# Kernel optimization log

Measured on AMD Instinct MI355X. Metric: run time of the kernel, lower is better.

The kernel has to match this reference:

```python
import jax, jax.numpy as jnp
import numpy as np

T, B, A, OBS = 128, 16, 32, 256
K, NACT, HID = 3, 9, 32


def setup_inputs() -> dict:
    key = jax.random.key(0)
    ks = jax.random.split(key, 12)
    sc = 0.1  # small init scale for stability
    d = {}
    d["x"] = jax.random.normal(ks[0], (T, B, A, OBS), jnp.float32)
    d["done"] = jax.random.randint(ks[1], (T, B), 0, 2, jnp.int32)
    d["actions"] = jax.random.randint(ks[2], (T, B, A, K), 0, NACT, jnp.int32)
    d["W1"] = sc * jax.random.normal(ks[3], (128, OBS), jnp.float32)
    d["b1"] = jnp.zeros((128,), jnp.float32)
    d["W2"] = sc * jax.random.normal(ks[4], (128, 128), jnp.float32)
    d["b2"] = jnp.zeros((128,), jnp.float32)
    d["W3"] = sc * jax.random.normal(ks[5], (64, 128), jnp.float32)
    d["b3"] = jnp.zeros((64,), jnp.float32)
    d["Wih"] = sc * jax.random.normal(ks[6], (4 * HID, 64), jnp.float32)
    d["Whh"] = sc * jax.random.normal(ks[7], (4 * HID, HID), jnp.float32)
    d["bih"] = jnp.zeros((4 * HID,), jnp.float32)
    d["bhh"] = jnp.zeros((4 * HID,), jnp.float32)
    d["Wh"] = sc * jax.random.normal(ks[8], (K, NACT, HID), jnp.float32)
    d["bh"] = jnp.zeros((K, NACT), jnp.float32)
    d["h0"] = jnp.zeros((B * A, HID), jnp.float32)
    d["c0"] = jnp.zeros((B * A, HID), jnp.float32)
    return d


def _forward(x, done, actions, W1, b1, W2, b2, W3, b3,
             Wih, Whh, bih, bhh, Wh, bh, h0, c0):
    # MLP trunk: n_obs -> 128 -> 128 -> 64 (tanh, tanh, linear)
    z = jnp.tanh(x @ W1.T + b1)
    z = jnp.tanh(z @ W2.T + b2)
    z = z @ W3.T + b3                       # [T, B, A, 64]
    zf = z.reshape(T, B * A, 64)
    # done[t] repeated per agent (repeat_interleave along batch*agent axis)
    done_f = jnp.repeat(done.astype(x.dtype), A, axis=1)  # [T, B*A]

    def step(carry, inp):
        h, c = carry
        zt, dt = inp                        # [B*A,64], [B*A]
        mask = (1.0 - dt)[:, None]
        h = h * mask
        c = c * mask
        gates = zt @ Wih.T + bih + h @ Whh.T + bhh  # [B*A, 4H]
        i, f, g, o = jnp.split(gates, 4, axis=-1)   # PyTorch gate order i,f,g,o
        i, f, o = jax.nn.sigmoid(i), jax.nn.sigmoid(f), jax.nn.sigmoid(o)
        g = jnp.tanh(g)
        c = f * c + i * g
        h = o * jnp.tanh(c)
        return (h, c), h

    (_, _), ys = jax.lax.scan(step, (h0, c0), (zf, done_f))
    y = ys.reshape(T, B, A, HID)
    # multi-head categorical logits: stacked heads [K, NACT, HID]
    logits = jnp.einsum('tbah,knh->tbakn', y, Wh) + bh  # [T,B,A,K,NACT]
    lp = jax.nn.log_softmax(logits, axis=-1)
    entropies = -jnp.sum(jnp.exp(lp) * lp, axis=-1)     # [T,B,A,K]
    alp = jnp.take_along_axis(lp, actions[..., None], axis=-1)[..., 0]  # [T,B,A,K]
    logprobs = jnp.prod(alp, axis=-1)  # faithful: product of per-head log-probs
    return logprobs, entropies


def reference(x, done, actions, W1, b1, W2, b2, W3, b3,
              Wih, Whh, bih, bhh, Wh, bh, h0, c0):
    logprobs, entropies = _forward(x, done, actions, W1, b1, W2, b2, W3, b3,
                                   Wih, Whh, bih, bhh, Wh, bh, h0, c0)
    return actions, logprobs, entropies
```

## Files before the change

kernel.cpp:

```cpp
#include <hip/hip_runtime.h>
#include <math.h>

namespace {
constexpr int Tn = 128, Bn = 16, An = 32, OBS = 256, Kh = 3, NACT = 9, HID = 32;
constexpr int TBA = Tn * Bn * An;
constexpr int BA  = Bn * An;
constexpr int OUT_LP  = TBA * Kh;
constexpr int OUT_ENT = TBA * Kh + TBA;
constexpr int NCHUNK = 32;
constexpr int CHUNKW = Tn / NCHUNK;

constexpr int W1_OFF  = 0;
constexpr int W2_OFF  = 32768;
constexpr int W3_OFF  = 49152;
constexpr int WIH_OFF = 57344;
constexpr int W16_TOT = 65536;

typedef __fp16   pk16x2 __attribute__((ext_vector_type(2)));
typedef _Float16 half8v __attribute__((ext_vector_type(8)));
typedef float    f32x4  __attribute__((ext_vector_type(4)));
}

__device__ __forceinline__ float fast_sig(float x) {
  return __builtin_amdgcn_rcpf(1.f + __expf(-x));
}
__device__ __forceinline__ float fast_tanh(float x) {
  return fmaf(2.f, fast_sig(2.f * x), -1.f);
}
__device__ __forceinline__ unsigned h2bits(pk16x2 h) {
  return __builtin_bit_cast(unsigned, h);
}
__device__ __forceinline__ pk16x2 bits2h(unsigned u) {
  return __builtin_bit_cast(pk16x2, u);
}
__device__ __forceinline__ int first_done_ge(unsigned long long dm0,
                                             unsigned long long dm1, int n) {
  unsigned long long m0 = (n < 64) ? (dm0 & (~0ull << n)) : 0ull;
  unsigned long long m1 = (n < 64) ? dm1 : (dm1 & (~0ull << (n - 64)));
  if (m0) return __builtin_ctzll(m0);
  if (m1) return 64 + __builtin_ctzll(m1);
  return 128;
}

__global__ __launch_bounds__(256) void cvtw_act_kernel(
    const float* __restrict__ W1, const float* __restrict__ W2,
    const float* __restrict__ W3, const float* __restrict__ Wih,
    _Float16* __restrict__ w16, const float* __restrict__ Whh,
    const int* __restrict__ done, _Float16* __restrict__ wt16,
    unsigned long long* __restrict__ dmask)
{
  const int bid = blockIdx.x;
  const int tid = threadIdx.x;
  if (bid < W16_TOT/256) {
    int i = bid * 256 + tid;
    float v;
    if (i < W2_OFF)       v = W1[i];
    else if (i < W3_OFF)  v = W2[i - W2_OFF];
    else if (i < WIH_OFF) v = W3[i - W3_OFF];
    else                  v = Wih[i - WIH_OFF];
    w16[i] = (_Float16)v;
  } else {
    for (int i = tid; i < 4096; i += 256) {
      int tl = i >> 9, rem = i & 511, l = rem >> 3, j = rem & 7;
      int gate = 16*tl + (l & 15);
      int unit = ((l >> 4) << 3) + j;
      wt16[i] = (_Float16)Whh[gate*HID + unit];
    }
    if (tid < 64) {
#pragma unroll
      for (int b = 0; b < Bn; ++b) {
        unsigned long long m0 = __ballot(done[tid*Bn + b] != 0);
        unsigned long long m1 = __ballot(done[(tid + 64)*Bn + b] != 0);
        if (tid == 0) { dmask[2*b] = m0; dmask[2*b + 1] = m1; }
      }
    }
  }
}

template<int ROWS, int WSTR>
__device__ __forceinline__ void stage_wh(const _Float16* __restrict__ Wg, int kofs,
                                         _Float16* __restrict__ wt, int tid)
{
#pragma unroll
  for (int it = 0; it < ROWS/64; ++it) {
    int idx = tid + it*512;
    int o = idx >> 3, g8 = idx & 7;
    *(half8v*)&wt[o*72 + g8*8] =
        *(const half8v*)&Wg[(size_t)o*WSTR + kofs + g8*8];
  }
}

template<int NOC, int XSTR>
__device__ __forceinline__ void mfma_slab(const _Float16* __restrict__ xsrc,
                                          const _Float16* __restrict__ wt,
                                          int rA, int ln, int quad, f32x4 acc[8])
{
#pragma unroll
  for (int kc = 0; kc < 2; ++kc) {
    half8v a = *(const half8v*)&xsrc[rA*XSTR + kc*32 + quad*8];
#pragma unroll
    for (int oc = 0; oc < NOC; ++oc) {
      half8v b = *(const half8v*)&wt[(oc*16 + ln)*72 + kc*32 + quad*8];
      acc[oc] = __builtin_amdgcn_mfma_f32_16x16x32_f16(a, b, acc[oc], 0, 0, 0);
    }
  }
}

template<int NOC>
__device__ __forceinline__ void mfma_regA(half8v a0, half8v a1,
                                          const _Float16* __restrict__ wt,
                                          int ln, int quad, f32x4 acc[8])
{
#pragma unroll
  for (int oc = 0; oc < NOC; ++oc) {
    half8v b = *(const half8v*)&wt[(oc*16 + ln)*72 + quad*8];
    acc[oc] = __builtin_amdgcn_mfma_f32_16x16x32_f16(a0, b, acc[oc], 0, 0, 0);
  }
#pragma unroll
  for (int oc = 0; oc < NOC; ++oc) {
    half8v b = *(const half8v*)&wt[(oc*16 + ln)*72 + 32 + quad*8];
    acc[oc] = __builtin_amdgcn_mfma_f32_16x16x32_f16(a1, b, acc[oc], 0, 0, 0);
  }
}

__global__ __launch_bounds__(512, 4) void mlp_kernel(
    const float* __restrict__ x, const _Float16* __restrict__ w16,
    const float* __restrict__ b1, const float* __restrict__ b2,
    const float* __restrict__ b3, const float* __restrict__ bih,
    const float* __restrict__ bhh, uint2* __restrict__ G1q)
{
  __shared__ __align__(16) _Float16 wt0[128*72];
  __shared__ __align__(16) _Float16 wt1[128*72];
  __shared__ __align__(16) _Float16 act[128*136];
  const _Float16* W1h  = w16 + W1_OFF;
  const _Float16* W2h  = w16 + W2_OFF;
  const _Float16* W3h  = w16 + W3_OFF;
  const _Float16* Wihh = w16 + WIH_OFF;
  const int tid  = threadIdx.x;
  const int w    = tid >> 6;
  const int lane = tid & 63;
  const int ln   = lane & 15;
  const int quad = lane >> 4;
  const int rA   = 16*w + ln;
  const int r0   = 16*w + quad*4;
  const int R0   = blockIdx.x * 128;
  f32x4 acc[8];
  const float* xrow = &x[(size_t)(R0 + rA)*OBS + quad*8];

#define XLOAD(KT, U0, U1, U2, U3) {                                   \
    const float* xp_ = xrow + (KT)*64;                                \
    U0 = *(const float4*)(xp_);      U1 = *(const float4*)(xp_ + 4);  \
    U2 = *(const float4*)(xp_ + 32); U3 = *(const float4*)(xp_ + 36); }
#define XCVT(U0, U1, U2, U3, A0, A1) {                                         \
    A0 = (half8v){(_Float16)U0.x,(_Float16)U0.y,(_Float16)U0.z,(_Float16)U0.w, \
                  (_Float16)U1.x,(_Float16)U1.y,(_Float16)U1.z,(_Float16)U1.w};\
    A1 = (half8v){(_Float16)U2.x,(_Float16)U2.y,(_Float16)U2.z,(_Float16)U2.w, \
                  (_Float16)U3.x,(_Float16)U3.y,(_Float16)U3.z,(_Float16)U3.w}; }

  float4 u0, u1, u2, u3, v0, v1, v2, v3;
  half8v a0, a1;

  XLOAD(0, u0, u1, u2, u3);
  stage_wh<128, 256>(W1h, 0, wt0, tid);
#pragma unroll
  for (int oc = 0; oc < 8; ++oc) acc[oc] = (f32x4)0.f;
  __syncthreads();

  stage_wh<128, 256>(W1h, 64, wt1, tid);
  XLOAD(1, v0, v1, v2, v3);
  XCVT(u0, u1, u2, u3, a0, a1);
  mfma_regA<8>(a0, a1, wt0, ln, quad, acc);
  __syncthreads();

  stage_wh<128, 256>(W1h, 128, wt0, tid);
  XLOAD(2, u0, u1, u2, u3);
  XCVT(v0, v1, v2, v3, a0, a1);
  mfma_regA<8>(a0, a1, wt1, ln, quad, acc);
  __syncthreads();

  stage_wh<128, 256>(W1h, 192, wt1, tid);
  XLOAD(3, v0, v1, v2, v3);
  XCVT(u0, u1, u2, u3, a0, a1);
  mfma_regA<8>(a0, a1, wt0, ln, quad, acc);
  __syncthreads();

  stage_wh<128, 128>(W2h, 0, wt0, tid);
  XCVT(v0, v1, v2, v3, a0, a1);
  mfma_regA<8>(a0, a1, wt1, ln, quad, acc);
  __syncthreads();

#pragma unroll
  for (int oc = 0; oc < 8; ++oc) {
    int o = oc*16 + ln;
    float bv = b1[o];
#pragma unroll
    for (int r = 0; r < 4; ++r)
      act[(r0 + r)*136 + o] = (_Float16)fast_tanh(acc[oc][r] + bv);
  }

#pragma unroll
  for (int oc = 0; oc < 8; ++oc) acc[oc] = (f32x4)0.f;
  stage_wh<128, 128>(W2h, 64, wt1, tid);
  mfma_slab<8, 136>(act, wt0, rA, ln, quad, acc);
  __syncthreads();

  stage_wh<64, 128>(W3h, 0, wt0, tid);
  mfma_slab<8, 136>(act + 64, wt1, rA, ln, quad, acc);
  __syncthreads();

#pragma unroll
  for (int oc = 0; oc < 8; ++oc) {
    int o = oc*16 + ln;
    float bv = b2[o];
#pragma unroll
    for (int r = 0; r < 4; ++r)
      act[(r0 + r)*136 + o] = (_Float16)fast_tanh(acc[oc][r] + bv);
  }

#pragma unroll
  for (int oc = 0; oc < 4; ++oc) acc[oc] = (f32x4)0.f;
  stage_wh<64, 128>(W3h, 64, wt1, tid);
  mfma_slab<4, 136>(act, wt0, rA, ln, quad, acc);
  __syncthreads();

  stage_wh<128, 64>(Wihh, 0, wt0, tid);
  mfma_slab<4, 136>(act + 64, wt1, rA, ln, quad, acc);
  __syncthreads();

#pragma unroll
  for (int oc = 0; oc < 4; ++oc) {
    int o = oc*16 + ln;
    float bv = b3[o];
#pragma unroll
    for (int r = 0; r < 4; ++r)
      act[(r0 + r)*136 + o] = (_Float16)(acc[oc][r] + bv);
  }

#pragma unroll
  for (int oc = 0; oc < 8; ++oc) acc[oc] = (f32x4)0.f;
  mfma_slab<8, 136>(act, wt0, rA, ln, quad, acc);
#pragma unroll
  for (int p = 0; p < 2; ++p) {
    int ui = p*16 + ln;
    float bi = bih[ui]      + bhh[ui];
    float bf = bih[ui + 32] + bhh[ui + 32];
    float bg = bih[ui + 64] + bhh[ui + 64];
    float bo = bih[ui + 96] + bhh[ui + 96];
#pragma unroll
    for (int r = 0; r < 4; ++r) {
      int n = R0 + r0 + r;
      uint2 q;
      q.x = h2bits(__builtin_amdgcn_cvt_pkrtz(acc[p  ][r] + bi, acc[p+4][r] + bg));
      q.y = h2bits(__builtin_amdgcn_cvt_pkrtz(acc[p+2][r] + bf, acc[p+6][r] + bo));
      G1q[(size_t)n*32 + ui] = q;
    }
  }
#undef XLOAD
#undef XCVT
}

__global__ __launch_bounds__(64) void lstm_kernel(
    const uint2* __restrict__ G1q, const _Float16* __restrict__ wt16,
    const unsigned long long* __restrict__ dmask,
    const float* __restrict__ h0, const float* __restrict__ c0,
    unsigned* __restrict__ Y16)
{
  static_assert(BA == 512 && NCHUNK == 32, "index math below assumes 512x32");
  const int lane = threadIdx.x;
  const int ln   = lane & 15;
  const int q    = lane >> 4;
  const int rg   = blockIdx.x & 31;
  const int ck   = blockIdx.x >> 5;
  const int R0   = rg * 16;
  const int b    = R0 >> 5;

  const unsigned long long dm0 = dmask[2*b];
  const unsigned long long dm1 = dmask[2*b + 1];

  const int s = (ck == 0) ? 0 : first_done_ge(dm0, dm1, ck * CHUNKW);
  const int e = (ck == NCHUNK - 1) ? Tn
                                   : first_done_ge(dm0, dm1, (ck + 1) * CHUNKW);
  if (s >= e) return;

  half8v wA0 = *(const half8v*)&wt16[0*512 + lane*8];
  half8v wA1 = *(const half8v*)&wt16[1*512 + lane*8];
  half8v wA2 = *(const half8v*)&wt16[2*512 + lane*8];
  half8v wA3 = *(const half8v*)&wt16[3*512 + lane*8];
  half8v wA4 = *(const half8v*)&wt16[4*512 + lane*8];
  half8v wA5 = *(const half8v*)&wt16[5*512 + lane*8];
  half8v wA6 = *(const half8v*)&wt16[6*512 + lane*8];
  half8v wA7 = *(const half8v*)&wt16[7*512 + lane*8];

  const float4 z4 = {0.f, 0.f, 0.f, 0.f};
  float4 cs0, cs1;
  unsigned w0, w1, w2, w3;
  if (ck == 0) {
    const float* hp = &h0[(size_t)(R0 + ln)*HID + 4*q];
    const float* cp = &c0[(size_t)(R0 + ln)*HID + 4*q];
    float4 ha = *(const float4*)hp;
    float4 hb = *(const float4*)(hp + 16);
    cs0 = *(const float4*)cp;
    cs1 = *(const float4*)(cp + 16);
    w0 = h2bits(__builtin_amdgcn_cvt_pkrtz(ha.x, ha.y));
    w1 = h2bits(__builtin_amdgcn_cvt_pkrtz(ha.z, ha.w));
    w2 = h2bits(__builtin_amdgcn_cvt_pkrtz(hb.x, hb.y));
    w3 = h2bits(__builtin_amdgcn_cvt_pkrtz(hb.z, hb.w));
  } else {
    cs0 = z4; cs1 = z4;
    w0 = w1 = w2 = w3 = 0u;
  }

  const int aA = (ln + ((q & 1) << 5)) << 2;
  const int aB = aA + (16 << 2);
  const bool loq = (q < 2);

  const uint2* gb = G1q + ((size_t)(R0 + ln) * 32 + 4*q);
  const size_t gstep = (size_t)BA * 32;

#define LOADG(T, A0, A1, A2, A3)                                  \
  { const uint2* p_ = gb + (size_t)(T) * gstep;                   \
    A0 = *(const uint4*)(p_);      A1 = *(const uint4*)(p_ + 2);  \
    A2 = *(const uint4*)(p_ + 16); A3 = *(const uint4*)(p_ + 18); }

  uint4 rc0, rc1, rc2, rc3;
  LOADG(s, rc0, rc1, rc2, rc3);

  for (int t = s; t < e; ++t) {
    int tn = (t + 1 < e) ? t + 1 : e - 1;
    uint4 rn0, rn1, rn2, rn3;
    LOADG(tn, rn0, rn1, rn2, rn3);

    unsigned long long dbit = (t < 64) ? (dm0 >> t) : (dm1 >> (t - 64));
    unsigned b0, b1, b2, b3;
    if (dbit & 1ull) {
      b0 = b1 = b2 = b3 = 0u;
      cs0 = z4; cs1 = z4;
    } else {
      unsigned e0 = (unsigned)__builtin_amdgcn_ds_bpermute(aA, (int)w0);
      unsigned e1 = (unsigned)__builtin_amdgcn_ds_bpermute(aA, (int)w1);
      unsigned e2 = (unsigned)__builtin_amdgcn_ds_bpermute(aA, (int)w2);
      unsigned e3 = (unsigned)__builtin_amdgcn_ds_bpermute(aA, (int)w3);
      unsigned o0 = (unsigned)__builtin_amdgcn_ds_bpermute(aB, (int)w0);
      unsigned o1 = (unsigned)__builtin_amdgcn_ds_bpermute(aB, (int)w1);
      unsigned o2 = (unsigned)__builtin_amdgcn_ds_bpermute(aB, (int)w2);
      unsigned o3 = (unsigned)__builtin_amdgcn_ds_bpermute(aB, (int)w3);
      b0 = loq ? e0 : e2;  b1 = loq ? e1 : e3;
      b2 = loq ? o0 : o2;  b3 = loq ? o1 : o3;
    }
    uint4 bu; bu.x = b0; bu.y = b1; bu.z = b2; bu.w = b3;
    half8v B = __builtin_bit_cast(half8v, bu);

    f32x4 ci0, cf0, cg0, co0, ci1, cf1, cg1, co1;
    {
      pk16x2 ig, fo;
      ig = bits2h(rc0.x); fo = bits2h(rc0.y);
      ci0[0] = ig.x; cg0[0] = ig.y; cf0[0] = fo.x; co0[0] = fo.y;
      ig = bits2h(rc0.z); fo = bits2h(rc0.w);
      ci0[1] = ig.x; cg0[1] = ig.y; cf0[1] = fo.x; co0[1] = fo.y;
      ig = bits2h(rc1.x); fo = bits2h(rc1.y);
      ci0[2] = ig.x; cg0[2] = ig.y; cf0[2] = fo.x; co0[2] = fo.y;
      ig = bits2h(rc1.z); fo = bits2h(rc1.w);
      ci0[3] = ig.x; cg0[3] = ig.y; cf0[3] = fo.x; co0[3] = fo.y;
      ig = bits2h(rc2.x); fo = bits2h(rc2.y);
      ci1[0] = ig.x; cg1[0] = ig.y; cf1[0] = fo.x; co1[0] = fo.y;
      ig = bits2h(rc2.z); fo = bits2h(rc2.w);
      ci1[1] = ig.x; cg1[1] = ig.y; cf1[1] = fo.x; co1[1] = fo.y;
      ig = bits2h(rc3.x); fo = bits2h(rc3.y);
      ci1[2] = ig.x; cg1[2] = ig.y; cf1[2] = fo.x; co1[2] = fo.y;
      ig = bits2h(rc3.z); fo = bits2h(rc3.w);
      ci1[3] = ig.x; cg1[3] = ig.y; cf1[3] = fo.x; co1[3] = fo.y;
    }

    f32x4 ai0 = __builtin_amdgcn_mfma_f32_16x16x32_f16(wA0, B, ci0, 0, 0, 0);
    f32x4 ai1 = __builtin_amdgcn_mfma_f32_16x16x32_f16(wA1, B, ci1, 0, 0, 0);
    f32x4 af0 = __builtin_amdgcn_mfma_f32_16x16x32_f16(wA2, B, cf0, 0, 0, 0);
    f32x4 af1 = __builtin_amdgcn_mfma_f32_16x16x32_f16(wA3, B, cf1, 0, 0, 0);
    f32x4 ag0 = __builtin_amdgcn_mfma_f32_16x16x32_f16(wA4, B, cg0, 0, 0, 0);
    f32x4 ag1 = __builtin_amdgcn_mfma_f32_16x16x32_f16(wA5, B, cg1, 0, 0, 0);
    f32x4 ao0 = __builtin_amdgcn_mfma_f32_16x16x32_f16(wA6, B, co0, 0, 0, 0);
    f32x4 ao1 = __builtin_amdgcn_mfma_f32_16x16x32_f16(wA7, B, co1, 0, 0, 0);

    f32x4 hva, hvb;
#pragma unroll
    for (int r = 0; r < 4; ++r) {
      float iv = fast_sig(ai0[r]);
      float fv = fast_sig(af0[r]);
      float gv = fast_tanh(ag0[r]);
      float ov = fast_sig(ao0[r]);
      float cc = fmaf(fv, cs0[r], iv * gv);
      cs0[r] = cc;
      hva[r] = ov * fast_tanh(cc);
    }
#pragma unroll
    for (int r = 0; r < 4; ++r) {
      float iv = fast_sig(ai1[r]);
      float fv = fast_sig(af1[r]);
      float gv = fast_tanh(ag1[r]);
      float ov = fast_sig(ao1[r]);
      float cc = fmaf(fv, cs1[r], iv * gv);
      cs1[r] = cc;
      hvb[r] = ov * fast_tanh(cc);
    }

    w0 = h2bits(__builtin_amdgcn_cvt_pkrtz(hva[0], hva[1]));
    w1 = h2bits(__builtin_amdgcn_cvt_pkrtz(hva[2], hva[3]));
    w2 = h2bits(__builtin_amdgcn_cvt_pkrtz(hvb[0], hvb[1]));
    w3 = h2bits(__builtin_amdgcn_cvt_pkrtz(hvb[2], hvb[3]));
    unsigned* yb = &Y16[((size_t)t*BA + R0 + ln)*16 + 2*q];
    uint2 ya; ya.x = w0; ya.y = w1;
    uint2 yc; yc.x = w2; yc.y = w3;
    *(uint2*)yb       = ya;
    *(uint2*)(yb + 8) = yc;

    rc0 = rn0; rc1 = rn1; rc2 = rn2; rc3 = rn3;
  }
#undef LOADG
}

__global__ __launch_bounds__(256) void head_kernel(
    const unsigned* __restrict__ Y16, const float* __restrict__ Wh,
    const float* __restrict__ bh, const int* __restrict__ actions,
    float* __restrict__ out)
{
  __shared__ __align__(16) float whs[27*32];
  __shared__ float bhs[32];
  const int tid = threadIdx.x;
  const int R0 = blockIdx.x * 256;
  for (int i = tid; i < 27*32; i += 256) whs[i] = Wh[i];
  if (tid < 27) bhs[tid] = bh[tid];
  const int row = R0 + tid;
  float yv[32];
#pragma unroll
  for (int i4 = 0; i4 < 4; ++i4) {
    uint4 yw = *(const uint4*)&Y16[(size_t)row*16 + i4*4];
    pk16x2 p0 = bits2h(yw.x), p1 = bits2h(yw.y), p2 = bits2h(yw.z), p3 = bits2h(yw.w);
    yv[i4*8+0] = (float)p0.x; yv[i4*8+1] = (float)p0.y;
    yv[i4*8+2] = (float)p1.x; yv[i4*8+3] = (float)p1.y;
    yv[i4*8+4] = (float)p2.x; yv[i4*8+5] = (float)p2.y;
    yv[i4*8+6] = (float)p3.x; yv[i4*8+7] = (float)p3.y;
  }
  __syncthreads();
  float l[27];
#pragma unroll
  for (int m = 0; m < 27; ++m) {
    float a = bhs[m];
#pragma unroll
    for (int k4 = 0; k4 < 8; ++k4) {
      float4 w4 = *(const float4*)&whs[m*32 + k4*4];
      a = fmaf(yv[k4*4+0], w4.x, a);
      a = fmaf(yv[k4*4+1], w4.y, a);
      a = fmaf(yv[k4*4+2], w4.z, a);
      a = fmaf(yv[k4*4+3], w4.w, a);
    }
    l[m] = a;
  }
  float logprob = 1.0f;
#pragma unroll
  for (int kk = 0; kk < 3; ++kk) {
    float mx = l[kk*9];
#pragma unroll
    for (int n = 1; n < 9; ++n) mx = fmaxf(mx, l[kk*9+n]);
    float s = 0.f;
#pragma unroll
    for (int n = 0; n < 9; ++n) s += __expf(l[kk*9+n] - mx);
    float lse = mx + __logf(s);
    float ent = 0.f;
#pragma unroll
    for (int n = 0; n < 9; ++n) {
      float lp = l[kk*9+n] - lse;
      ent -= __expf(lp) * lp;
    }
    int a = actions[row*3 + kk];
    out[row*3 + kk] = (float)a;
    float alp = 0.f;
#pragma unroll
    for (int n = 0; n < 9; ++n) alp = (a == n) ? (l[kk*9+n] - lse) : alp;
    logprob *= alp;
    out[OUT_ENT + row*3 + kk] = ent;
  }
  out[OUT_LP + row] = logprob;
}

extern "C" void kernel_launch(void* const* d_in, const int* in_sizes, int n_in,
                              void* d_out, int out_size, void* d_ws, size_t ws_size,
                              hipStream_t stream)
{
  const float* x       = (const float*)d_in[0];
  const int*   done    = (const int*)  d_in[1];
  const int*   actions = (const int*)  d_in[2];
  const float* W1  = (const float*)d_in[3];
  const float* b1  = (const float*)d_in[4];
  const float* W2  = (const float*)d_in[5];
  const float* b2  = (const float*)d_in[6];
  const float* W3  = (const float*)d_in[7];
  const float* b3  = (const float*)d_in[8];
  const float* Wih = (const float*)d_in[9];
  const float* Whh = (const float*)d_in[10];
  const float* bih = (const float*)d_in[11];
  const float* bhh = (const float*)d_in[12];
  const float* Wh  = (const float*)d_in[13];
  const float* bh  = (const float*)d_in[14];
  const float* h0  = (const float*)d_in[15];
  const float* c0  = (const float*)d_in[16];
  float* out = (float*)d_out;

  uint2* G1q = (uint2*)d_ws;
  unsigned* Y16 = (unsigned*)(G1q + (size_t)TBA*32);
  _Float16* W16 = (_Float16*)(Y16 + (size_t)TBA*16);
  _Float16* WT16 = W16 + W16_TOT;
  unsigned long long* Dm = (unsigned long long*)(WT16 + 4096);

  cvtw_act_kernel<<<W16_TOT/256 + 1, 256, 0, stream>>>(
      W1, W2, W3, Wih, W16, Whh, done, WT16, Dm);
  mlp_kernel<<<TBA/128, 512, 0, stream>>>(x, W16, b1, b2, b3, bih, bhh, G1q);
  lstm_kernel<<<32 * NCHUNK, 64, 0, stream>>>(G1q, WT16, Dm, h0, c0, Y16);
  head_kernel<<<TBA/256, 256, 0, stream>>>(Y16, Wh, bh, actions, out);
}
```

Before: 168.6 us.

## Fuse weight conversion into MLP and head computation into LSTM kernel

The separate weight-conversion kernel goes away: the MLP kernel now converts fp32 weights to fp16 as it stages them into shared memory, and the LSTM kernel builds its Whh fragments and done masks directly from the inputs. The head kernel is folded into the LSTM step, which computes logits with two extra MFMAs on the freshly built h fragment and does log-softmax, entropy and the action log-prob product through cross-lane shuffles. This removes two launches and the fp16 Y round-trip through global memory. In exchange, every MLP block repeats the fp32 weight loads and conversion, and the head work lands on the serial recurrence critical path.

```diff
diff --git a/kernel.cpp b/kernel.cpp
--- a/kernel.cpp
+++ b/kernel.cpp
@@ -10,12 +10,6 @@
 constexpr int NCHUNK = 32;
 constexpr int CHUNKW = Tn / NCHUNK;
 
-constexpr int W1_OFF  = 0;
-constexpr int W2_OFF  = 32768;
-constexpr int W3_OFF  = 49152;
-constexpr int WIH_OFF = 57344;
-constexpr int W16_TOT = 65536;
-
 typedef __fp16   pk16x2 __attribute__((ext_vector_type(2)));
 typedef _Float16 half8v __attribute__((ext_vector_type(8)));
 typedef float    f32x4  __attribute__((ext_vector_type(4)));
@@ -41,52 +35,39 @@
   if (m1) return 64 + __builtin_ctzll(m1);
   return 128;
 }
-
-__global__ __launch_bounds__(256) void cvtw_act_kernel(
-    const float* __restrict__ W1, const float* __restrict__ W2,
-    const float* __restrict__ W3, const float* __restrict__ Wih,
-    _Float16* __restrict__ w16, const float* __restrict__ Whh,
-    const int* __restrict__ done, _Float16* __restrict__ wt16,
-    unsigned long long* __restrict__ dmask)
-{
-  const int bid = blockIdx.x;
-  const int tid = threadIdx.x;
-  if (bid < W16_TOT/256) {
-    int i = bid * 256 + tid;
-    float v;
-    if (i < W2_OFF)       v = W1[i];
-    else if (i < W3_OFF)  v = W2[i - W2_OFF];
-    else if (i < WIH_OFF) v = W3[i - W3_OFF];
-    else                  v = Wih[i - WIH_OFF];
-    w16[i] = (_Float16)v;
-  } else {
-    for (int i = tid; i < 4096; i += 256) {
-      int tl = i >> 9, rem = i & 511, l = rem >> 3, j = rem & 7;
-      int gate = 16*tl + (l & 15);
-      int unit = ((l >> 4) << 3) + j;
-      wt16[i] = (_Float16)Whh[gate*HID + unit];
-    }
-    if (tid < 64) {
-#pragma unroll
-      for (int b = 0; b < Bn; ++b) {
-        unsigned long long m0 = __ballot(done[tid*Bn + b] != 0);
-        unsigned long long m1 = __ballot(done[(tid + 64)*Bn + b] != 0);
-        if (tid == 0) { dmask[2*b] = m0; dmask[2*b + 1] = m1; }
-      }
-    }
-  }
+__device__ __forceinline__ void bmax3(float& m0, float& m1, float& m2,
+                                      int km, float v) {
+  m0 = (km == 0) ? fmaxf(m0, v) : m0;
+  m1 = (km == 1) ? fmaxf(m1, v) : m1;
+  m2 = (km == 2) ? fmaxf(m2, v) : m2;
+}
+__device__ __forceinline__ void badd3(float& s0, float& s1, float& s2,
+                                      int km, float v) {
+  s0 += (km == 0) ? v : 0.f;
+  s1 += (km == 1) ? v : 0.f;
+  s2 += (km == 2) ? v : 0.f;
+}
+__device__ __forceinline__ float bsel3(float x0, float x1, float x2, int km) {
+  return (km == 0) ? x0 : ((km == 1) ? x1 : x2);
+}
+__device__ __forceinline__ int bseli3(int x0, int x1, int x2, int km) {
+  return (km == 0) ? x0 : ((km == 1) ? x1 : x2);
 }
 
 template<int ROWS, int WSTR>
-__device__ __forceinline__ void stage_wh(const _Float16* __restrict__ Wg, int kofs,
-                                         _Float16* __restrict__ wt, int tid)
+__device__ __forceinline__ void stage_whf(const float* __restrict__ Wg, int kofs,
+                                          _Float16* __restrict__ wt, int tid)
 {
 #pragma unroll
   for (int it = 0; it < ROWS/64; ++it) {
     int idx = tid + it*512;
     int o = idx >> 3, g8 = idx & 7;
-    *(half8v*)&wt[o*72 + g8*8] =
-        *(const half8v*)&Wg[(size_t)o*WSTR + kofs + g8*8];
+    const float* p = &Wg[(size_t)o*WSTR + kofs + g8*8];
+    float4 c0 = *(const float4*)p;
+    float4 c1 = *(const float4*)(p + 4);
+    half8v hv = { (_Float16)c0.x, (_Float16)c0.y, (_Float16)c0.z, (_Float16)c0.w,
+                  (_Float16)c1.x, (_Float16)c1.y, (_Float16)c1.z, (_Float16)c1.w };
+    *(half8v*)&wt[o*72 + g8*8] = hv;
   }
 }
 
@@ -124,7 +105,9 @@
 }
 
 __global__ __launch_bounds__(512, 4) void mlp_kernel(
-    const float* __restrict__ x, const _Float16* __restrict__ w16,
+    const float* __restrict__ x,
+    const float* __restrict__ W1, const float* __restrict__ W2,
+    const float* __restrict__ W3, const float* __restrict__ Wih,
     const float* __restrict__ b1, const float* __restrict__ b2,
     const float* __restrict__ b3, const float* __restrict__ bih,
     const float* __restrict__ bhh, uint2* __restrict__ G1q)
@@ -132,10 +115,6 @@
   __shared__ __align__(16) _Float16 wt0[128*72];
   __shared__ __align__(16) _Float16 wt1[128*72];
   __shared__ __align__(16) _Float16 act[128*136];
-  const _Float16* W1h  = w16 + W1_OFF;
-  const _Float16* W2h  = w16 + W2_OFF;
-  const _Float16* W3h  = w16 + W3_OFF;
-  const _Float16* Wihh = w16 + WIH_OFF;
   const int tid  = threadIdx.x;
   const int w    = tid >> 6;
   const int lane = tid & 63;
@@ -161,30 +140,30 @@
   half8v a0, a1;
 
   XLOAD(0, u0, u1, u2, u3);
-  stage_wh<128, 256>(W1h, 0, wt0, tid);
+  stage_whf<128, 256>(W1, 0, wt0, tid);
 #pragma unroll
   for (int oc = 0; oc < 8; ++oc) acc[oc] = (f32x4)0.f;
   __syncthreads();
 
-  stage_wh<128, 256>(W1h, 64, wt1, tid);
+  stage_whf<128, 256>(W1, 64, wt1, tid);
   XLOAD(1, v0, v1, v2, v3);
   XCVT(u0, u1, u2, u3, a0, a1);
   mfma_regA<8>(a0, a1, wt0, ln, quad, acc);
   __syncthreads();
 
-  stage_wh<128, 256>(W1h, 128, wt0, tid);
+  stage_whf<128, 256>(W1, 128, wt0, tid);
   XLOAD(2, u0, u1, u2, u3);
   XCVT(v0, v1, v2, v3, a0, a1);
   mfma_regA<8>(a0, a1, wt1, ln, quad, acc);
   __syncthreads();
 
-  stage_wh<128, 256>(W1h, 192, wt1, tid);
+  stage_whf<128, 256>(W1, 192, wt1, tid);
   XLOAD(3, v0, v1, v2, v3);
   XCVT(u0, u1, u2, u3, a0, a1);
   mfma_regA<8>(a0, a1, wt0, ln, quad, acc);
   __syncthreads();
 
-  stage_wh<128, 128>(W2h, 0, wt0, tid);
+  stage_whf<128, 128>(W2, 0, wt0, tid);
   XCVT(v0, v1, v2, v3, a0, a1);
   mfma_regA<8>(a0, a1, wt1, ln, quad, acc);
   __syncthreads();
@@ -200,11 +179,11 @@
 
 #pragma unroll
   for (int oc = 0; oc < 8; ++oc) acc[oc] = (f32x4)0.f;
-  stage_wh<128, 128>(W2h, 64, wt1, tid);
+  stage_whf<128, 128>(W2, 64, wt1, tid);
   mfma_slab<8, 136>(act, wt0, rA, ln, quad, acc);
   __syncthreads();
 
-  stage_wh<64, 128>(W3h, 0, wt0, tid);
+  stage_whf<64, 128>(W3, 0, wt0, tid);
   mfma_slab<8, 136>(act + 64, wt1, rA, ln, quad, acc);
   __syncthreads();
 
@@ -219,11 +198,11 @@
 
 #pragma unroll
   for (int oc = 0; oc < 4; ++oc) acc[oc] = (f32x4)0.f;
-  stage_wh<64, 128>(W3h, 64, wt1, tid);
+  stage_whf<64, 128>(W3, 64, wt1, tid);
   mfma_slab<4, 136>(act, wt0, rA, ln, quad, acc);
   __syncthreads();
 
-  stage_wh<128, 64>(Wihh, 0, wt0, tid);
+  stage_whf<128, 64>(Wih, 0, wt0, tid);
   mfma_slab<4, 136>(act + 64, wt1, rA, ln, quad, acc);
   __syncthreads();
 
@@ -260,10 +239,11 @@
 }
 
 __global__ __launch_bounds__(64) void lstm_kernel(
-    const uint2* __restrict__ G1q, const _Float16* __restrict__ wt16,
-    const unsigned long long* __restrict__ dmask,
+    const uint2* __restrict__ G1q, const float* __restrict__ Whh,
+    const float* __restrict__ Wh, const float* __restrict__ bh,
+    const int* __restrict__ done, const int* __restrict__ actions,
     const float* __restrict__ h0, const float* __restrict__ c0,
-    unsigned* __restrict__ Y16)
+    float* __restrict__ out)
 {
   static_assert(BA == 512 && NCHUNK == 32, "index math below assumes 512x32");
   const int lane = threadIdx.x;
@@ -274,22 +254,60 @@
   const int R0   = rg * 16;
   const int b    = R0 >> 5;
 
-  const unsigned long long dm0 = dmask[2*b];
-  const unsigned long long dm1 = dmask[2*b + 1];
+  const unsigned long long dm0 = __ballot(done[lane*Bn + b] != 0);
+  const unsigned long long dm1 = __ballot(done[(lane + 64)*Bn + b] != 0);
 
   const int s = (ck == 0) ? 0 : first_done_ge(dm0, dm1, ck * CHUNKW);
   const int e = (ck == NCHUNK - 1) ? Tn
                                    : first_done_ge(dm0, dm1, (ck + 1) * CHUNKW);
   if (s >= e) return;
 
-  half8v wA0 = *(const half8v*)&wt16[0*512 + lane*8];
-  half8v wA1 = *(const half8v*)&wt16[1*512 + lane*8];
-  half8v wA2 = *(const half8v*)&wt16[2*512 + lane*8];
-  half8v wA3 = *(const half8v*)&wt16[3*512 + lane*8];
-  half8v wA4 = *(const half8v*)&wt16[4*512 + lane*8];
-  half8v wA5 = *(const half8v*)&wt16[5*512 + lane*8];
-  half8v wA6 = *(const half8v*)&wt16[6*512 + lane*8];
-  half8v wA7 = *(const half8v*)&wt16[7*512 + lane*8];
+#define WFRAG(DST, ROWBASE, SRC, STRIDE, SCALE) {                              \
+    const float* p_ = &(SRC)[(size_t)((ROWBASE) + ln)*(STRIDE) + q*8];         \
+    float4 c0_ = *(const float4*)p_;                                           \
+    float4 c1_ = *(const float4*)(p_ + 4);                                     \
+    DST = (half8v){                                                            \
+      (_Float16)(c0_.x*(SCALE)), (_Float16)(c0_.y*(SCALE)),                    \
+      (_Float16)(c0_.z*(SCALE)), (_Float16)(c0_.w*(SCALE)),                    \
+      (_Float16)(c1_.x*(SCALE)), (_Float16)(c1_.y*(SCALE)),                    \
+      (_Float16)(c1_.z*(SCALE)), (_Float16)(c1_.w*(SCALE))}; }
+
+  half8v wA0, wA1, wA2, wA3, wA4, wA5, wA6, wA7;
+  WFRAG(wA0,   0, Whh, HID, 1.f)  WFRAG(wA1,  16, Whh, HID, 1.f)
+  WFRAG(wA2,  32, Whh, HID, 1.f)  WFRAG(wA3,  48, Whh, HID, 1.f)
+  WFRAG(wA4,  64, Whh, HID, 1.f)  WFRAG(wA5,  80, Whh, HID, 1.f)
+  WFRAG(wA6,  96, Whh, HID, 1.f)  WFRAG(wA7, 112, Whh, HID, 1.f)
+
+  half8v whA0, whA1;
+  WFRAG(whA0, 0, Wh, HID, 1.f)
+  {
+    int row = 16 + ln;
+    int rc  = (row < 27) ? row : 0;
+    float zf = (row < 27) ? 1.f : 0.f;
+    const float* p_ = &Wh[(size_t)rc*HID + q*8];
+    float4 c0_ = *(const float4*)p_;
+    float4 c1_ = *(const float4*)(p_ + 4);
+    whA1 = (half8v){
+      (_Float16)(c0_.x*zf), (_Float16)(c0_.y*zf),
+      (_Float16)(c0_.z*zf), (_Float16)(c0_.w*zf),
+      (_Float16)(c1_.x*zf), (_Float16)(c1_.y*zf),
+      (_Float16)(c1_.z*zf), (_Float16)(c1_.w*zf)};
+  }
+
+  f32x4 bc0, bc1;
+#pragma unroll
+  for (int r = 0; r < 4; ++r) {
+    int m0 = 4*q + r;
+    int m1 = 16 + 4*q + r;
+    bc0[r] = bh[m0];
+    bc1[r] = (m1 < 27) ? bh[m1] : -1e30f;
+  }
+
+#define KOF(M, K, O) int K = (M)/9; K = (K > 2) ? 2 : K; const int O = (M) - 9*K;
+  const int mA = 4*q, mB = 16 + 4*q;
+  KOF(mA+0, kA0, oA0) KOF(mA+1, kA1, oA1) KOF(mA+2, kA2, oA2) KOF(mA+3, kA3, oA3)
+  KOF(mB+0, kB0, oB0) KOF(mB+1, kB1, oB1) KOF(mB+2, kB2, oB2) KOF(mB+3, kB3, oB3)
+#undef KOF
 
   const float4 z4 = {0.f, 0.f, 0.f, 0.f};
   float4 cs0, cs1;
@@ -314,6 +332,27 @@
   const int aB = aA + (16 << 2);
   const bool loq = (q < 2);
 
+#define BBUILD(DST) {                                                      \
+    unsigned e0_ = (unsigned)__builtin_amdgcn_ds_bpermute(aA, (int)w0);    \
+    unsigned e1_ = (unsigned)__builtin_amdgcn_ds_bpermute(aA, (int)w1);    \
+    unsigned e2_ = (unsigned)__builtin_amdgcn_ds_bpermute(aA, (int)w2);    \
+    unsigned e3_ = (unsigned)__builtin_amdgcn_ds_bpermute(aA, (int)w3);    \
+    unsigned o0_ = (unsigned)__builtin_amdgcn_ds_bpermute(aB, (int)w0);    \
+    unsigned o1_ = (unsigned)__builtin_amdgcn_ds_bpermute(aB, (int)w1);    \
+    unsigned o2_ = (unsigned)__builtin_amdgcn_ds_bpermute(aB, (int)w2);    \
+    unsigned o3_ = (unsigned)__builtin_amdgcn_ds_bpermute(aB, (int)w3);    \
+    uint4 bu_;                                                             \
+    bu_.x = loq ? e0_ : e2_;  bu_.y = loq ? e1_ : e3_;                     \
+    bu_.z = loq ? o0_ : o2_;  bu_.w = loq ? o1_ : o3_;                     \
+    DST = __builtin_bit_cast(half8v, bu_); }
+
+  half8v Bprev;
+  if (ck == 0) { BBUILD(Bprev) }
+  else {
+    uint4 zz; zz.x = zz.y = zz.z = zz.w = 0u;
+    Bprev = __builtin_bit_cast(half8v, zz);
+  }
+
   const uint2* gb = G1q + ((size_t)(R0 + ln) * 32 + 4*q);
   const size_t gstep = (size_t)BA * 32;
 
@@ -330,25 +369,17 @@
     uint4 rn0, rn1, rn2, rn3;
     LOADG(tn, rn0, rn1, rn2, rn3);
 
+    const int rowG = t*BA + R0 + ln;
+    const int* ap = actions + (size_t)rowG*3;
+    int a0 = ap[0], a1 = ap[1], a2 = ap[2];
+
     unsigned long long dbit = (t < 64) ? (dm0 >> t) : (dm1 >> (t - 64));
-    unsigned b0, b1, b2, b3;
+    half8v Buse = Bprev;
     if (dbit & 1ull) {
-      b0 = b1 = b2 = b3 = 0u;
+      uint4 zz; zz.x = zz.y = zz.z = zz.w = 0u;
+      Buse = __builtin_bit_cast(half8v, zz);
       cs0 = z4; cs1 = z4;
-    } else {
-      unsigned e0 = (unsigned)__builtin_amdgcn_ds_bpermute(aA, (int)w0);
-      unsigned e1 = (unsigned)__builtin_amdgcn_ds_bpermute(aA, (int)w1);
-      unsigned e2 = (unsigned)__builtin_amdgcn_ds_bpermute(aA, (int)w2);
-      unsigned e3 = (unsigned)__builtin_amdgcn_ds_bpermute(aA, (int)w3);
-      unsigned o0 = (unsigned)__builtin_amdgcn_ds_bpermute(aB, (int)w0);
-      unsigned o1 = (unsigned)__builtin_amdgcn_ds_bpermute(aB, (int)w1);
-      unsigned o2 = (unsigned)__builtin_amdgcn_ds_bpermute(aB, (int)w2);
-      unsigned o3 = (unsigned)__builtin_amdgcn_ds_bpermute(aB, (int)w3);
-      b0 = loq ? e0 : e2;  b1 = loq ? e1 : e3;
-      b2 = loq ? o0 : o2;  b3 = loq ? o1 : o3;
-    }
-    uint4 bu; bu.x = b0; bu.y = b1; bu.z = b2; bu.w = b3;
-    half8v B = __builtin_bit_cast(half8v, bu);
+    }
 
     f32x4 ci0, cf0, cg0, co0, ci1, cf1, cg1, co1;
     {
@@ -371,14 +402,14 @@
       ci1[3] = ig.x; cg1[3] = ig.y; cf1[3] = fo.x; co1[3] = fo.y;
     }
 
-    f32x4 ai0 = __builtin_amdgcn_mfma_f32_16x16x32_f16(wA0, B, ci0, 0, 0, 0);
-    f32x4 ai1 = __builtin_amdgcn_mfma_f32_16x16x32_f16(wA1, B, ci1, 0, 0, 0);
-    f32x4 af0 = __builtin_amdgcn_mfma_f32_16x16x32_f16(wA2, B, cf0, 0, 0, 0);
-    f32x4 af1 = __builtin_amdgcn_mfma_f32_16x16x32_f16(wA3, B, cf1, 0, 0, 0);
-    f32x4 ag0 = __builtin_amdgcn_mfma_f32_16x16x32_f16(wA4, B, cg0, 0, 0, 0);
-    f32x4 ag1 = __builtin_amdgcn_mfma_f32_16x16x32_f16(wA5, B, cg1, 0, 0, 0);
-    f32x4 ao0 = __builtin_amdgcn_mfma_f32_16x16x32_f16(wA6, B, co0, 0, 0, 0);
-    f32x4 ao1 = __builtin_amdgcn_mfma_f32_16x16x32_f16(wA7, B, co1, 0, 0, 0);
+    f32x4 ai0 = __builtin_amdgcn_mfma_f32_16x16x32_f16(wA0, Buse, ci0, 0, 0, 0);
+    f32x4 ai1 = __builtin_amdgcn_mfma_f32_16x16x32_f16(wA1, Buse, ci1, 0, 0, 0);
+    f32x4 af0 = __builtin_amdgcn_mfma_f32_16x16x32_f16(wA2, Buse, cf0, 0, 0, 0);
+    f32x4 af1 = __builtin_amdgcn_mfma_f32_16x16x32_f16(wA3, Buse, cf1, 0, 0, 0);
+    f32x4 ag0 = __builtin_amdgcn_mfma_f32_16x16x32_f16(wA4, Buse, cg0, 0, 0, 0);
+    f32x4 ag1 = __builtin_amdgcn_mfma_f32_16x16x32_f16(wA5, Buse, cg1, 0, 0, 0);
+    f32x4 ao0 = __builtin_amdgcn_mfma_f32_16x16x32_f16(wA6, Buse, co0, 0, 0, 0);
+    f32x4 ao1 = __builtin_amdgcn_mfma_f32_16x16x32_f16(wA7, Buse, co1, 0, 0, 0);
 
     f32x4 hva, hvb;
 #pragma unroll
@@ -406,79 +437,75 @@
     w1 = h2bits(__builtin_amdgcn_cvt_pkrtz(hva[2], hva[3]));
     w2 = h2bits(__builtin_amdgcn_cvt_pkrtz(hvb[0], hvb[1]));
     w3 = h2bits(__builtin_amdgcn_cvt_pkrtz(hvb[2], hvb[3]));
-    unsigned* yb = &Y16[((size_t)t*BA + R0 + ln)*16 + 2*q];
-    uint2 ya; ya.x = w0; ya.y = w1;
-    uint2 yc; yc.x = w2; yc.y = w3;
-    *(uint2*)yb       = ya;
-    *(uint2*)(yb + 8) = yc;
+    BBUILD(Bprev)
+
+    f32x4 lh0 = __builtin_amdgcn_mfma_f32_16x16x32_f16(whA0, Bprev, bc0, 0, 0, 0);
+    f32x4 lh1 = __builtin_amdgcn_mfma_f32_16x16x32_f16(whA1, Bprev, bc1, 0, 0, 0);
+
+    float mx0 = -1e30f, mx1 = -1e30f, mx2 = -1e30f;
+    bmax3(mx0, mx1, mx2, kA0, lh0[0]); bmax3(mx0, mx1, mx2, kA1, lh0[1]);
+    bmax3(mx0, mx1, mx2, kA2, lh0[2]); bmax3(mx0, mx1, mx2, kA3, lh0[3]);
+    bmax3(mx0, mx1, mx2, kB0, lh1[0]); bmax3(mx0, mx1, mx2, kB1, lh1[1]);
+    bmax3(mx0, mx1, mx2, kB2, lh1[2]); bmax3(mx0, mx1, mx2, kB3, lh1[3]);
+    mx0 = fmaxf(mx0, __shfl_xor(mx0, 16)); mx0 = fmaxf(mx0, __shfl_xor(mx0, 32));
+    mx1 = fmaxf(mx1, __shfl_xor(mx1, 16)); mx1 = fmaxf(mx1, __shfl_xor(mx1, 32));
+    mx2 = fmaxf(mx2, __shfl_xor(mx2, 16)); mx2 = fmaxf(mx2, __shfl_xor(mx2, 32));
+
+    float ev0 = __expf(lh0[0] - bsel3(mx0, mx1, mx2, kA0));
+    float ev1 = __expf(lh0[1] - bsel3(mx0, mx1, mx2, kA1));
+    float ev2 = __expf(lh0[2] - bsel3(mx0, mx1, mx2, kA2));
+    float ev3 = __expf(lh0[3] - bsel3(mx0, mx1, mx2, kA3));
+    float ev4 = __expf(lh1[0] - bsel3(mx0, mx1, mx2, kB0));
+    float ev5 = __expf(lh1[1] - bsel3(mx0, mx1, mx2, kB1));
+    float ev6 = __expf(lh1[2] - bsel3(mx0, mx1, mx2, kB2));
+    float ev7 = __expf(lh1[3] - bsel3(mx0, mx1, mx2, kB3));
+    float s0 = 0.f, s1 = 0.f, s2 = 0.f;
+    badd3(s0, s1, s2, kA0, ev0); badd3(s0, s1, s2, kA1, ev1);
+    badd3(s0, s1, s2, kA2, ev2); badd3(s0, s1, s2, kA3, ev3);
+    badd3(s0, s1, s2, kB0, ev4); badd3(s0, s1, s2, kB1, ev5);
+    badd3(s0, s1, s2, kB2, ev6); badd3(s0, s1, s2, kB3, ev7);
+    s0 += __shfl_xor(s0, 16); s0 += __shfl_xor(s0, 32);
+    s1 += __shfl_xor(s1, 16); s1 += __shfl_xor(s1, 32);
+    s2 += __shfl_xor(s2, 16); s2 += __shfl_xor(s2, 32);
+    float lse0 = mx0 + __logf(s0);
+    float lse1 = mx1 + __logf(s1);
+    float lse2 = mx2 + __logf(s2);
+    float sc0 = __expf(mx0 - lse0);
+    float sc1 = __expf(mx1 - lse1);
+    float sc2 = __expf(mx2 - lse2);
+
+    float en0 = 0.f, en1 = 0.f, en2 = 0.f;
+    float pl = 1.f;
+#define HSLOT(LV, EV, KM, OM) {                                \
+      float lse_ = bsel3(lse0, lse1, lse2, KM);                \
+      float lp_  = (LV) - lse_;                                \
+      float p_   = (EV) * bsel3(sc0, sc1, sc2, KM);            \
+      badd3(en0, en1, en2, KM, -p_ * lp_);                     \
+      int a_ = bseli3(a0, a1, a2, KM);                         \
+      pl = ((OM) == a_) ? pl * lp_ : pl; }
+    HSLOT(lh0[0], ev0, kA0, oA0) HSLOT(lh0[1], ev1, kA1, oA1)
+    HSLOT(lh0[2], ev2, kA2, oA2) HSLOT(lh0[3], ev3, kA3, oA3)
+    HSLOT(lh1[0], ev4, kB0, oB0) HSLOT(lh1[1], ev5, kB1, oB1)
+    HSLOT(lh1[2], ev6, kB2, oB2) HSLOT(lh1[3], ev7, kB3, oB3)
+#undef HSLOT
+    en0 += __shfl_xor(en0, 16); en0 += __shfl_xor(en0, 32);
+    en1 += __shfl_xor(en1, 16); en1 += __shfl_xor(en1, 32);
+    en2 += __shfl_xor(en2, 16); en2 += __shfl_xor(en2, 32);
+    pl  *= __shfl_xor(pl, 16);  pl  *= __shfl_xor(pl, 32);
+
+    if (q == 0) {
+      float* ob = out + (size_t)rowG*3;
+      ob[0] = (float)a0; ob[1] = (float)a1; ob[2] = (float)a2;
+      float* eb = out + OUT_ENT + (size_t)rowG*3;
+      eb[0] = en0; eb[1] = en1; eb[2] = en2;
+      out[OUT_LP + rowG] = pl;
+    }
 
     rc0 = rn0; rc1 = rn1; rc2 = rn2; rc3 = rn3;
   }
 #undef LOADG
-}
-
-__global__ __launch_bounds__(256) void head_kernel(
-    const unsigned* __restrict__ Y16, const float* __restrict__ Wh,
-    const float* __restrict__ bh, const int* __restrict__ actions,
-    float* __restrict__ out)
-{
-  __shared__ __align__(16) float whs[27*32];
-  __shared__ float bhs[32];
-  const int tid = threadIdx.x;
-  const int R0 = blockIdx.x * 256;
-  for (int i = tid; i < 27*32; i += 256) whs[i] = Wh[i];
-  if (tid < 27) bhs[tid] = bh[tid];
-  const int row = R0 + tid;
-  float yv[32];
-#pragma unroll
-  for (int i4 = 0; i4 < 4; ++i4) {
-    uint4 yw = *(const uint4*)&Y16[(size_t)row*16 + i4*4];
-    pk16x2 p0 = bits2h(yw.x), p1 = bits2h(yw.y), p2 = bits2h(yw.z), p3 = bits2h(yw.w);
-    yv[i4*8+0] = (float)p0.x; yv[i4*8+1] = (float)p0.y;
-    yv[i4*8+2] = (float)p1.x; yv[i4*8+3] = (float)p1.y;
-    yv[i4*8+4] = (float)p2.x; yv[i4*8+5] = (float)p2.y;
-    yv[i4*8+6] = (float)p3.x; yv[i4*8+7] = (float)p3.y;
-  }
-  __syncthreads();
-  float l[27];
-#pragma unroll
-  for (int m = 0; m < 27; ++m) {
-    float a = bhs[m];
-#pragma unroll
-    for (int k4 = 0; k4 < 8; ++k4) {
-      float4 w4 = *(const float4*)&whs[m*32 + k4*4];
-      a = fmaf(yv[k4*4+0], w4.x, a);
-      a = fmaf(yv[k4*4+1], w4.y, a);
-      a = fmaf(yv[k4*4+2], w4.z, a);
-      a = fmaf(yv[k4*4+3], w4.w, a);
-    }
-    l[m] = a;
-  }
-  float logprob = 1.0f;
-#pragma unroll
-  for (int kk = 0; kk < 3; ++kk) {
-    float mx = l[kk*9];
-#pragma unroll
-    for (int n = 1; n < 9; ++n) mx = fmaxf(mx, l[kk*9+n]);
-    float s = 0.f;
-#pragma unroll
-    for (int n = 0; n < 9; ++n) s += __expf(l[kk*9+n] - mx);
-    float lse = mx + __logf(s);
-    float ent = 0.f;
-#pragma unroll
-    for (int n = 0; n < 9; ++n) {
-      float lp = l[kk*9+n] - lse;
-      ent -= __expf(lp) * lp;
-    }
-    int a = actions[row*3 + kk];
-    out[row*3 + kk] = (float)a;
-    float alp = 0.f;
-#pragma unroll
-    for (int n = 0; n < 9; ++n) alp = (a == n) ? (l[kk*9+n] - lse) : alp;
-    logprob *= alp;
-    out[OUT_ENT + row*3 + kk] = ent;
-  }
-  out[OUT_LP + row] = logprob;
+#undef BBUILD
+#undef WFRAG
 }
 
 extern "C" void kernel_launch(void* const* d_in, const int* in_sizes, int n_in,
@@ -505,14 +532,9 @@
   float* out = (float*)d_out;
 
   uint2* G1q = (uint2*)d_ws;
-  unsigned* Y16 = (unsigned*)(G1q + (size_t)TBA*32);
-  _Float16* W16 = (_Float16*)(Y16 + (size_t)TBA*16);
-  _Float16* WT16 = W16 + W16_TOT;
-  unsigned long long* Dm = (unsigned long long*)(WT16 + 4096);
-
-  cvtw_act_kernel<<<W16_TOT/256 + 1, 256, 0, stream>>>(
-      W1, W2, W3, Wih, W16, Whh, done, WT16, Dm);
-  mlp_kernel<<<TBA/128, 512, 0, stream>>>(x, W16, b1, b2, b3, bih, bhh, G1q);
-  lstm_kernel<<<32 * NCHUNK, 64, 0, stream>>>(G1q, WT16, Dm, h0, c0, Y16);
-  head_kernel<<<TBA/256, 256, 0, stream>>>(Y16, Wh, bh, actions, out);
-}
+
+  mlp_kernel<<<TBA/128, 512, 0, stream>>>(
+      x, W1, W2, W3, Wih, b1, b2, b3, bih, bhh, G1q);
+  lstm_kernel<<<32 * NCHUNK, 64, 0, stream>>>(
+      G1q, Whh, Wh, bh, done, actions, h0, c0, out);
+}
```

Result: no change. 168.2 us (-0.3%).
